# Kernel tuning notes

Hardware: AMD Instinct MI355X
Metric: run time of the kernel (lower is better)

The kernel has to match this reference:

```python
import jax, jax.numpy as jnp
import numpy as np

MARGIN = 0.2
LAMBDA_LSE = 6.0
LAMBDA_SOFTMAX = 9.0
EPS = 1e-8


def setup_inputs() -> dict:
    key = jax.random.key(0)
    k1, k2, k3 = jax.random.split(key, 3)
    I, R, W, D = 128, 36, 24, 512
    images = jax.random.normal(k1, (I, R, D), dtype=jnp.float32)
    captions = jax.random.normal(k2, (I, W, D), dtype=jnp.float32)
    # ragged caption lengths in [4, 24]
    cap_lens = 4 + jax.random.randint(k3, (I,), 0, W - 3, dtype=jnp.int32)
    return {"images": images, "captions": captions, "cap_lens": cap_lens}


def _scan_t2i_loss(images, captions, cap_lens):
    # images: [I, R, D]; captions: [C, W, D]; cap_lens: [C]
    C, W, D = captions.shape
    wmask = jnp.arange(W)[None, :] < cap_lens[:, None]          # [C, W] valid-word mask

    # raw attention: bmm(context=images, query^T=caption) -> [C, I, R, W]
    attn = jnp.einsum('ird,cwd->cirw', images, captions)
    # clipped_l2norm: LeakyReLU(0.1) then l2-normalize over word axis;
    # zero padded words so norms match the per-caption sliced computation
    a = jnp.where(attn > 0, attn, 0.1 * attn) * wmask[:, None, None, :]
    a = a / (jnp.sqrt(jnp.sum(a * a, axis=3, keepdims=True)) + EPS)
    # softmax over regions (sourceL) with temperature lambda_softmax
    s = jax.nn.softmax(a * LAMBDA_SOFTMAX, axis=2)              # [C, I, R, W]
    # weighted context per word: [C, I, W, D]
    wei = jnp.einsum('cirw,ird->ciwd', s, images)

    cap = captions[:, None, :, :]                               # [C, 1, W, D]
    num = jnp.sum(cap * wei, axis=-1)                           # [C, I, W]
    den = jnp.clip(jnp.linalg.norm(cap, axis=-1) * jnp.linalg.norm(wei, axis=-1), EPS)
    cos = num / den                                             # [C, I, W]

    # LogSumExp aggregation over valid words
    neg = jnp.finfo(cos.dtype).min
    logits = jnp.where(wmask[:, None, :], cos * LAMBDA_LSE, neg)
    row_sim = jax.nn.logsumexp(logits, axis=-1) / LAMBDA_LSE    # [C, I]
    scores = row_sim.T                                          # [I, C] (image x caption)

    diag = jnp.diag(scores)[:, None]                            # [I, 1]
    cost_s = jnp.clip(MARGIN + scores - diag, 0.0)
    cost_im = jnp.clip(MARGIN + scores - diag.T, 0.0)
    eye = jnp.eye(scores.shape[0], dtype=bool)
    cost_s = jnp.where(eye, 0.0, cost_s)
    cost_im = jnp.where(eye, 0.0, cost_im)
    # max_violation=True: hardest negatives
    cost_s = jnp.max(cost_s, axis=1)
    cost_im = jnp.max(cost_im, axis=0)
    return jnp.sum(cost_s) + jnp.sum(cost_im)


def reference(images, captions, cap_lens):
    return _scan_t2i_loss(images, captions, cap_lens)
```

## Files before the change

### kernel.cpp

```cpp
#include <hip/hip_runtime.h>
#include <math.h>

#define I_N 128
#define C_N 128
#define R_N 36
#define W_N 24
#define D_N 512
#define M_N (I_N * R_N)
#define N_N (C_N * W_N)

typedef __attribute__((ext_vector_type(8))) short bf16x8;
typedef __attribute__((ext_vector_type(4))) float f32x4;
typedef __attribute__((ext_vector_type(8))) unsigned short u16x8;
typedef _Float16 f16x2 __attribute__((ext_vector_type(2)));
typedef __fp16 h16x2 __attribute__((ext_vector_type(2)));

__device__ inline float bf2f(unsigned short u) {
    return __uint_as_float(((unsigned int)u) << 16);
}
__device__ inline unsigned short f2bf(float f) {
    unsigned int u = __float_as_uint(f);
    u = (u + 0x7FFFu + ((u >> 16) & 1u)) >> 16;
    return (unsigned short)u;
}
__device__ inline void gload_lds16(const void* g, void* l) {
    __builtin_amdgcn_global_load_lds(
        (const __attribute__((address_space(1))) void*)g,
        (__attribute__((address_space(3))) void*)l, 16, 0, 0);
}

#if __has_builtin(__builtin_amdgcn_fdot2)
__device__ inline float fdot2f(f16x2 a, f16x2 b, float c) {
    return __builtin_amdgcn_fdot2(__builtin_bit_cast(h16x2, a),
                                  __builtin_bit_cast(h16x2, b), c, false);
}
#else
__device__ inline float fdot2f(f16x2 a, f16x2 b, float c) {
    return c + (float)a[0] * (float)b[0] + (float)a[1] * (float)b[1];
}
#endif

#if __has_builtin(__builtin_amdgcn_cvt_pkrtz)
__device__ inline f16x2 pkf16(float a, float b) {
    return __builtin_bit_cast(f16x2, __builtin_amdgcn_cvt_pkrtz(a, b));
}
#else
__device__ inline f16x2 pkf16(float a, float b) {
    f16x2 v; v[0] = (_Float16)a; v[1] = (_Float16)b; return v;
}
#endif

__global__ __launch_bounds__(256) void convert_kernel(const float* __restrict__ images,
                                                      const float* __restrict__ captions,
                                                      unsigned short* __restrict__ imgbf,
                                                      unsigned short* __restrict__ capbf,
                                                      float* __restrict__ capn) {
    const int bid = blockIdx.x;
    if (bid < 1152) {
        int idx = bid * 256 + threadIdx.x;
        float4 v0 = *(const float4*)(images + (size_t)idx * 8);
        float4 v1 = *(const float4*)(images + (size_t)idx * 8 + 4);
        u16x8 o;
        o[0] = f2bf(v0.x); o[1] = f2bf(v0.y); o[2] = f2bf(v0.z); o[3] = f2bf(v0.w);
        o[4] = f2bf(v1.x); o[5] = f2bf(v1.y); o[6] = f2bf(v1.z); o[7] = f2bf(v1.w);
        *(u16x8*)(imgbf + (size_t)idx * 8) = o;
    } else {
        const int crow = (bid - 1152) * 4 + (threadIdx.x >> 6);
        const int lane = threadIdx.x & 63;
        const float* p = captions + (size_t)crow * D_N + lane * 8;
        float4 v0 = *(const float4*)p;
        float4 v1 = *(const float4*)(p + 4);
        u16x8 o;
        o[0] = f2bf(v0.x); o[1] = f2bf(v0.y); o[2] = f2bf(v0.z); o[3] = f2bf(v0.w);
        o[4] = f2bf(v1.x); o[5] = f2bf(v1.y); o[6] = f2bf(v1.z); o[7] = f2bf(v1.w);
        *(u16x8*)(capbf + (size_t)crow * D_N + lane * 8) = o;
        float s = v0.x*v0.x + v0.y*v0.y + v0.z*v0.z + v0.w*v0.w
                + v1.x*v1.x + v1.y*v1.y + v1.z*v1.z + v1.w*v1.w;
        #pragma unroll
        for (int off = 32; off > 0; off >>= 1) s += __shfl_down(s, off);
        if (lane == 0) capn[crow] = sqrtf(s);
    }
}

__global__ __launch_bounds__(256) void gram_kernel(const float* __restrict__ images,
                                                   float* __restrict__ G) {
    __shared__ float tile[R_N][68];
    const int i = blockIdx.x;
    const float* img = images + (size_t)i * R_N * D_N;
    const int tid = threadIdx.x;
    const int t1 = (tid / 12) * 3;
    const int t2 = (tid % 12) * 3;
    const bool active = tid < 144;
    float acc[3][3] = {{0.f,0.f,0.f},{0.f,0.f,0.f},{0.f,0.f,0.f}};
    for (int k0 = 0; k0 < D_N; k0 += 64) {
        for (int idx = tid; idx < R_N * 16; idx += 256) {
            int r = idx / 16, k4 = idx % 16;
            float4 v = *(const float4*)(img + (size_t)r * D_N + k0 + k4 * 4);
            *(float4*)&tile[r][k4 * 4] = v;
        }
        __syncthreads();
        if (active) {
            #pragma unroll
            for (int k = 0; k < 64; k += 4) {
                float4 a0 = *(const float4*)&tile[t1 + 0][k];
                float4 a1 = *(const float4*)&tile[t1 + 1][k];
                float4 a2 = *(const float4*)&tile[t1 + 2][k];
                float4 b0 = *(const float4*)&tile[t2 + 0][k];
                float4 b1 = *(const float4*)&tile[t2 + 1][k];
                float4 b2 = *(const float4*)&tile[t2 + 2][k];
                acc[0][0] += a0.x*b0.x + a0.y*b0.y + a0.z*b0.z + a0.w*b0.w;
                acc[0][1] += a0.x*b1.x + a0.y*b1.y + a0.z*b1.z + a0.w*b1.w;
                acc[0][2] += a0.x*b2.x + a0.y*b2.y + a0.z*b2.z + a0.w*b2.w;
                acc[1][0] += a1.x*b0.x + a1.y*b0.y + a1.z*b0.z + a1.w*b0.w;
                acc[1][1] += a1.x*b1.x + a1.y*b1.y + a1.z*b1.z + a1.w*b1.w;
                acc[1][2] += a1.x*b2.x + a1.y*b2.y + a1.z*b2.z + a1.w*b2.w;
                acc[2][0] += a2.x*b0.x + a2.y*b0.y + a2.z*b0.z + a2.w*b0.w;
                acc[2][1] += a2.x*b1.x + a2.y*b1.y + a2.z*b1.z + a2.w*b1.w;
                acc[2][2] += a2.x*b2.x + a2.y*b2.y + a2.z*b2.z + a2.w*b2.w;
            }
        }
        __syncthreads();
    }
    if (active) {
        float* gp = G + (size_t)i * R_N * R_N;
        #pragma unroll
        for (int a = 0; a < 3; ++a)
            #pragma unroll
            for (int b = 0; b < 3; ++b)
                gp[(t1 + a) * R_N + (t2 + b)] = acc[a][b];
    }
}

#define BM 128
#define BN 128
#define BK 64
#define KT (D_N / BK)
#define GX (M_N / BM)
#define GY (N_N / BN)

__global__ __launch_bounds__(256) void attn_gemm_kernel(const unsigned short* __restrict__ A,
                                                        const unsigned short* __restrict__ B,
                                                        unsigned short* __restrict__ attn) {
    __shared__ unsigned short AsBuf[2][BM * BK];
    __shared__ unsigned short BsBuf[2][BN * BK];
    const int flat = blockIdx.y * GX + blockIdx.x;
    const int nf = (flat & 7) * (GX * GY / 8) + (flat >> 3);
    const int m0 = (nf % GX) * BM;
    const int n0 = (nf / GX) * BN;
    const int tid = threadIdx.x;
    const int lane = tid & 63;
    const int wid = tid >> 6;
    const int wr = wid >> 1, wc = wid & 1;
    const int fr = lane & 15;
    const int fk = lane >> 4;

    const int srow = tid >> 3;
    const int sslot = (tid & 7) ^ (srow & 7);
    const unsigned short* srcA = A + (size_t)(m0 + srow) * D_N + sslot * 8;
    const unsigned short* srcB = B + (size_t)(n0 + srow) * D_N + sslot * 8;
    const int ldst = tid * 16;

    f32x4 acc[4][4];
    #pragma unroll
    for (int m = 0; m < 4; ++m)
        #pragma unroll
        for (int n = 0; n < 4; ++n) acc[m][n] = (f32x4){0.f, 0.f, 0.f, 0.f};

    #define STAGE(t, buf)                                                          \
        {                                                                          \
            const unsigned short* _a = srcA + (t) * BK;                            \
            const unsigned short* _b = srcB + (t) * BK;                            \
            _Pragma("unroll")                                                      \
            for (int r = 0; r < 4; ++r) {                                          \
                gload_lds16(_a + (size_t)r * 32 * D_N, (char*)AsBuf[buf] + r * 4096 + ldst); \
                gload_lds16(_b + (size_t)r * 32 * D_N, (char*)BsBuf[buf] + r * 4096 + ldst); \
            }                                                                      \
        }

    STAGE(0, 0)
    STAGE(1, 1)
    asm volatile("s_waitcnt vmcnt(8)" ::: "memory");
    __builtin_amdgcn_sched_barrier(0);
    __builtin_amdgcn_s_barrier();
    __builtin_amdgcn_sched_barrier(0);

    #pragma unroll
    for (int t = 0; t < KT; ++t) {
        const int cur = t & 1;
        const unsigned short* As = AsBuf[cur];
        const unsigned short* Bs = BsBuf[cur];
        #pragma unroll
        for (int ks = 0; ks < 2; ++ks) {
            bf16x8 af[4], bfr[4];
            #pragma unroll
            for (int m = 0; m < 4; ++m) {
                int rl = wr * 64 + m * 16 + fr;
                int byt = rl * 128 + ((ks * 64 + fk * 16) ^ ((fr & 7) << 4));
                af[m] = *(const bf16x8*)((const char*)As + byt);
            }
            #pragma unroll
            for (int n = 0; n < 4; ++n) {
                int rl = wc * 64 + n * 16 + fr;
                int byt = rl * 128 + ((ks * 64 + fk * 16) ^ ((fr & 7) << 4));
                bfr[n] = *(const bf16x8*)((const char*)Bs + byt);
            }
            #pragma unroll
            for (int m = 0; m < 4; ++m)
                #pragma unroll
                for (int n = 0; n < 4; ++n)
                    acc[m][n] = __builtin_amdgcn_mfma_f32_16x16x32_bf16(af[m], bfr[n], acc[m][n], 0, 0, 0);
        }
        __builtin_amdgcn_sched_barrier(0);
        __builtin_amdgcn_s_barrier();
        __builtin_amdgcn_sched_barrier(0);
        if (t + 2 < KT) STAGE(t + 2, cur)
        if (t + 1 < KT) {
            if (t + 2 < KT) {
                asm volatile("s_waitcnt vmcnt(8)" ::: "memory");
            } else {
                asm volatile("s_waitcnt vmcnt(0)" ::: "memory");
            }
            __builtin_amdgcn_sched_barrier(0);
            __builtin_amdgcn_s_barrier();
            __builtin_amdgcn_sched_barrier(0);
        }
    }
    #undef STAGE

    #pragma unroll
    for (int m = 0; m < 4; ++m) {
        #pragma unroll
        for (int n = 0; n < 4; ++n) {
            #pragma unroll
            for (int j = 0; j < 4; ++j) {
                int row = m0 + wr * 64 + m * 16 + fk * 4 + j;
                int col = n0 + wc * 64 + n * 16 + fr;
                int i = row / R_N, r = row - i * R_N;
                int c = col / W_N, w = col - c * W_N;
                attn[(((size_t)i * C_N + c) * R_N + r) * W_N + w] = f2bf(acc[m][n][j]);
            }
        }
    }
}

#define CG 16
#define SCL9 12.98425537f

__global__ __launch_bounds__(192) void score_kernel(const unsigned short* __restrict__ attn,
                                                    const float* __restrict__ G,
                                                    const float* __restrict__ capn,
                                                    const int* __restrict__ cap_lens,
                                                    float* __restrict__ scores) {
    __shared__ unsigned short stage[CG * R_N * W_N];
    __shared__ unsigned int gsh2[R_N][20];
    __shared__ float scl_sh[CG * R_N];
    __shared__ float red[CG][W_N];
    __shared__ int len_sh[CG];
    const int i = blockIdx.x;
    const int c0 = blockIdx.y * CG;
    const int tid = threadIdx.x;

    if (tid < CG) len_sh[tid] = cap_lens[c0 + tid];
    const unsigned short* at = attn + ((size_t)i * C_N + c0) * R_N * W_N;
    for (int ch = tid; ch < CG * R_N * W_N / 8; ch += 192)
        *(u16x8*)&stage[ch * 8] = *(const u16x8*)(at + ch * 8);
    const float* gp = G + (size_t)i * R_N * R_N;
    for (int idx = tid; idx < R_N * 20; idx += 192) {
        int r = idx / 20, p = idx % 20;
        f16x2 v;
        if (p < 18) v = pkf16(gp[r * R_N + 2 * p], gp[r * R_N + 2 * p + 1]);
        else { v[0] = (_Float16)0.f; v[1] = (_Float16)0.f; }
        gsh2[r][p] = __builtin_bit_cast(unsigned int, v);
    }
    __syncthreads();

    for (int row = tid; row < CG * R_N; row += 192) {
        int cl = row / R_N;
        int len = len_sh[cl];
        const unsigned short* rp = &stage[row * W_N];
        u16x8 p0 = *(const u16x8*)&rp[0];
        u16x8 p1 = *(const u16x8*)&rp[8];
        u16x8 p2 = *(const u16x8*)&rp[16];
        float ss = 0.f;
        #pragma unroll
        for (int q = 0; q < 8; ++q) {
            float x0 = bf2f(p0[q]); x0 = x0 > 0.f ? x0 : 0.1f * x0; x0 = (q      < len) ? x0 : 0.f;
            float x1 = bf2f(p1[q]); x1 = x1 > 0.f ? x1 : 0.1f * x1; x1 = (q + 8  < len) ? x1 : 0.f;
            float x2 = bf2f(p2[q]); x2 = x2 > 0.f ? x2 : 0.1f * x2; x2 = (q + 16 < len) ? x2 : 0.f;
            ss += x0 * x0 + x1 * x1 + x2 * x2;
        }
        scl_sh[row] = SCL9 / (sqrtf(ss) + 1e-8f);
    }
    __syncthreads();

    {
        const int cl = tid / 12, w0 = (tid % 12) * 2;
        const int len = len_sh[cl];
        const bool va = w0 < len, vb = w0 + 1 < len;
        const unsigned short* sb = &stage[cl * R_N * W_N];
        const float* sclp = &scl_sh[cl * R_N];
        f16x2 epa[18], epb[18];
        float Z0 = 0.f, Z1 = 0.f, nu0 = 0.f, nu1 = 0.f;
        float ea_prev = 0.f, eb_prev = 0.f;
        #pragma unroll
        for (int r = 0; r < R_N; ++r) {
            unsigned int pr = *(const unsigned int*)&sb[r * W_N + w0];
            float ra = bf2f((unsigned short)(pr & 0xffffu));
            float rb = bf2f((unsigned short)(pr >> 16));
            float s = sclp[r];
            float xa = ra > 0.f ? ra : 0.1f * ra;
            float xb = rb > 0.f ? rb : 0.1f * rb;
            float la = va ? xa * s : 0.f;
            float lb = vb ? xb * s : 0.f;
            float ea = exp2f(la), eb = exp2f(lb);
            Z0 += ea; Z1 += eb;
            nu0 += ea * ra; nu1 += eb * rb;
            if (r & 1) {
                epa[r >> 1] = pkf16(ea_prev, ea);
                epb[r >> 1] = pkf16(eb_prev, eb);
            } else {
                ea_prev = ea; eb_prev = eb;
            }
        }
        float wna = 0.f, wnb = 0.f;
        #pragma unroll
        for (int r2 = 0; r2 < R_N; ++r2) {
            const uint4* g4 = (const uint4*)&gsh2[r2][0];
            uint4 q0 = g4[0], q1 = g4[1], q2 = g4[2], q3 = g4[3];
            uint2 q4 = *(const uint2*)&gsh2[r2][16];
            unsigned int gq[18] = {q0.x, q0.y, q0.z, q0.w,
                                   q1.x, q1.y, q1.z, q1.w,
                                   q2.x, q2.y, q2.z, q2.w,
                                   q3.x, q3.y, q3.z, q3.w,
                                   q4.x, q4.y};
            float t0a = 0.f, t0b = 0.f, t1a = 0.f, t1b = 0.f;
            #pragma unroll
            for (int p = 0; p < 18; ++p) {
                f16x2 g = __builtin_bit_cast(f16x2, gq[p]);
                if (p & 1) { t0b = fdot2f(g, epa[p], t0b); t1b = fdot2f(g, epb[p], t1b); }
                else       { t0a = fdot2f(g, epa[p], t0a); t1a = fdot2f(g, epb[p], t1a); }
            }
            float ta = t0a + t0b, tb = t1a + t1b;
            float e2a = (float)epa[r2 >> 1][r2 & 1];
            float e2b = (float)epb[r2 >> 1][r2 & 1];
            wna += ta * e2a;
            wnb += tb * e2b;
        }
        float iZ0 = 1.f / Z0, iZ1 = 1.f / Z1;
        float cna = capn[(c0 + cl) * W_N + w0];
        float cnb = capn[(c0 + cl) * W_N + w0 + 1];
        float dena = fmaxf(cna * sqrtf(fmaxf(wna, 0.f)) * iZ0, 1e-8f);
        float denb = fmaxf(cnb * sqrtf(fmaxf(wnb, 0.f)) * iZ1, 1e-8f);
        red[cl][w0]     = va ? (nu0 * iZ0) / dena * 6.0f : -3.4e38f;
        red[cl][w0 + 1] = vb ? (nu1 * iZ1) / denb * 6.0f : -3.4e38f;
    }
    __syncthreads();
    if (tid < CG) {
        float se = 0.f;
        #pragma unroll
        for (int w = 0; w < W_N; ++w) se += __expf(red[tid][w] - 6.0f);
        scores[(size_t)(c0 + tid) * I_N + i] = (__logf(se) + 6.0f) / 6.0f;
    }
}

__global__ __launch_bounds__(128) void final_kernel(const float* __restrict__ scores,
                                                    float* __restrict__ out) {
    __shared__ float diag[C_N];
    __shared__ float red[C_N];
    const int t = threadIdx.x;
    diag[t] = scores[t * C_N + t];
    __syncthreads();
    const float di = diag[t];
    float cs = 0.f, cim = 0.f;
    for (int k = 0; k < C_N; ++k) {
        if (k == t) continue;
        float vs = 0.2f + scores[k * C_N + t] - di;
        float vi = 0.2f + scores[t * C_N + k] - di;
        cs = fmaxf(cs, vs);
        cim = fmaxf(cim, vi);
    }
    red[t] = cs + cim;
    __syncthreads();
    #pragma unroll
    for (int off = 64; off > 0; off >>= 1) {
        if (t < off) red[t] += red[t + off];
        __syncthreads();
    }
    if (t == 0) out[0] = red[0];
}

extern "C" void kernel_launch(void* const* d_in, const int* in_sizes, int n_in,
                              void* d_out, int out_size, void* d_ws, size_t ws_size,
                              hipStream_t stream) {
    (void)in_sizes; (void)n_in; (void)out_size; (void)ws_size;
    const float* images = (const float*)d_in[0];
    const float* captions = (const float*)d_in[1];
    const int* cap_lens = (const int*)d_in[2];
    float* out = (float*)d_out;

    char* wsb = (char*)d_ws;
    size_t off = 0;
    auto alloc = [&](size_t bytes) -> char* {
        char* p = wsb + off;
        off += (bytes + 255) & ~(size_t)255;
        return p;
    };
    unsigned short* imgbf = (unsigned short*)alloc((size_t)M_N * D_N * 2);
    unsigned short* capbf = (unsigned short*)alloc((size_t)N_N * D_N * 2);
    float* Gw = (float*)alloc((size_t)I_N * R_N * R_N * 4);
    float* capn = (float*)alloc((size_t)C_N * W_N * 4);
    float* scores = (float*)alloc((size_t)C_N * I_N * 4);
    unsigned short* attn = (unsigned short*)alloc((size_t)I_N * C_N * R_N * W_N * 2);

    convert_kernel<<<1920, 256, 0, stream>>>(images, captions, imgbf, capbf, capn);
    gram_kernel<<<I_N, 256, 0, stream>>>(images, Gw);
    attn_gemm_kernel<<<dim3(GX, GY), 256, 0, stream>>>(imgbf, capbf, attn);
    score_kernel<<<dim3(I_N, C_N / CG), 192, 0, stream>>>(attn, Gw, capn, cap_lens, scores);
    final_kernel<<<1, 128, 0, stream>>>(scores, out);
}
```

Before: 129.6 us.

## Halve GEMM K-tile, raise occupancy, remap blocks, pre-pack Gram matrix as fp16

Halves the attention GEMM's K tile from 64 to 32, which halves LDS use, and adds a launch bound of 4 blocks per CU to raise occupancy. It also switches to a 1-D grid with an M-major block remap and a matching LDS swizzle. The Gram kernel now writes its result already packed as fp16 pairs, so the score kernel drops its shared-memory Gram staging and reads the packed rows straight from global memory. The trade-offs are more barriers per K step in the GEMM, possible register pressure from the occupancy bound, and uncached global reads in the score kernel's inner loop.

```diff
diff --git a/kernel.cpp b/kernel.cpp
--- a/kernel.cpp
+++ b/kernel.cpp
@@ -83,8 +83,9 @@
 }
 
 __global__ __launch_bounds__(256) void gram_kernel(const float* __restrict__ images,
-                                                   float* __restrict__ G) {
+                                                   unsigned int* __restrict__ G2) {
     __shared__ float tile[R_N][68];
+    __shared__ float gshf[R_N][R_N];
     const int i = blockIdx.x;
     const float* img = images + (size_t)i * R_N * D_N;
     const int tid = threadIdx.x;
@@ -122,31 +123,36 @@
         __syncthreads();
     }
     if (active) {
-        float* gp = G + (size_t)i * R_N * R_N;
         #pragma unroll
         for (int a = 0; a < 3; ++a)
             #pragma unroll
             for (int b = 0; b < 3; ++b)
-                gp[(t1 + a) * R_N + (t2 + b)] = acc[a][b];
+                gshf[t1 + a][t2 + b] = acc[a][b];
+    }
+    __syncthreads();
+    unsigned int* gp = G2 + (size_t)i * (R_N * 18);
+    for (int idx = tid; idx < R_N * 18; idx += 256) {
+        int r = idx / 18, p = idx % 18;
+        gp[idx] = __builtin_bit_cast(unsigned int, pkf16(gshf[r][2 * p], gshf[r][2 * p + 1]));
     }
 }
 
 #define BM 128
 #define BN 128
-#define BK 64
+#define BK 32
 #define KT (D_N / BK)
 #define GX (M_N / BM)
 #define GY (N_N / BN)
 
-__global__ __launch_bounds__(256) void attn_gemm_kernel(const unsigned short* __restrict__ A,
-                                                        const unsigned short* __restrict__ B,
-                                                        unsigned short* __restrict__ attn) {
+__global__ __launch_bounds__(256, 4) void attn_gemm_kernel(const unsigned short* __restrict__ A,
+                                                           const unsigned short* __restrict__ B,
+                                                           unsigned short* __restrict__ attn) {
     __shared__ unsigned short AsBuf[2][BM * BK];
     __shared__ unsigned short BsBuf[2][BN * BK];
-    const int flat = blockIdx.y * GX + blockIdx.x;
+    const int flat = blockIdx.x;
     const int nf = (flat & 7) * (GX * GY / 8) + (flat >> 3);
-    const int m0 = (nf % GX) * BM;
-    const int n0 = (nf / GX) * BN;
+    const int m0 = (nf / GY) * BM;
+    const int n0 = (nf % GY) * BN;
     const int tid = threadIdx.x;
     const int lane = tid & 63;
     const int wid = tid >> 6;
@@ -154,8 +160,8 @@
     const int fr = lane & 15;
     const int fk = lane >> 4;
 
-    const int srow = tid >> 3;
-    const int sslot = (tid & 7) ^ (srow & 7);
+    const int srow = tid >> 2;
+    const int sslot = (tid & 3) ^ (srow & 3);
     const unsigned short* srcA = A + (size_t)(m0 + srow) * D_N + sslot * 8;
     const unsigned short* srcB = B + (size_t)(n0 + srow) * D_N + sslot * 8;
     const int ldst = tid * 16;
@@ -166,20 +172,19 @@
         #pragma unroll
         for (int n = 0; n < 4; ++n) acc[m][n] = (f32x4){0.f, 0.f, 0.f, 0.f};
 
-    #define STAGE(t, buf)                                                          \
-        {                                                                          \
-            const unsigned short* _a = srcA + (t) * BK;                            \
-            const unsigned short* _b = srcB + (t) * BK;                            \
-            _Pragma("unroll")                                                      \
-            for (int r = 0; r < 4; ++r) {                                          \
-                gload_lds16(_a + (size_t)r * 32 * D_N, (char*)AsBuf[buf] + r * 4096 + ldst); \
-                gload_lds16(_b + (size_t)r * 32 * D_N, (char*)BsBuf[buf] + r * 4096 + ldst); \
-            }                                                                      \
+    #define STAGE(t, buf)                                                              \
+        {                                                                              \
+            const unsigned short* _a = srcA + (t) * BK;                                \
+            const unsigned short* _b = srcB + (t) * BK;                                \
+            gload_lds16(_a, (char*)AsBuf[buf] + ldst);                                 \
+            gload_lds16(_a + (size_t)64 * D_N, (char*)AsBuf[buf] + 4096 + ldst);       \
+            gload_lds16(_b, (char*)BsBuf[buf] + ldst);                                 \
+            gload_lds16(_b + (size_t)64 * D_N, (char*)BsBuf[buf] + 4096 + ldst);       \
         }
 
     STAGE(0, 0)
     STAGE(1, 1)
-    asm volatile("s_waitcnt vmcnt(8)" ::: "memory");
+    asm volatile("s_waitcnt vmcnt(4)" ::: "memory");
     __builtin_amdgcn_sched_barrier(0);
     __builtin_amdgcn_s_barrier();
     __builtin_amdgcn_sched_barrier(0);
@@ -189,34 +194,31 @@
         const int cur = t & 1;
         const unsigned short* As = AsBuf[cur];
         const unsigned short* Bs = BsBuf[cur];
-        #pragma unroll
-        for (int ks = 0; ks < 2; ++ks) {
-            bf16x8 af[4], bfr[4];
+        bf16x8 af[4], bfr[4];
+        #pragma unroll
+        for (int m = 0; m < 4; ++m) {
+            int rl = wr * 64 + m * 16 + fr;
+            int byt = rl * 64 + ((fk ^ (fr & 3)) << 4);
+            af[m] = *(const bf16x8*)((const char*)As + byt);
+        }
+        #pragma unroll
+        for (int n = 0; n < 4; ++n) {
+            int rl = wc * 64 + n * 16 + fr;
+            int byt = rl * 64 + ((fk ^ (fr & 3)) << 4);
+            bfr[n] = *(const bf16x8*)((const char*)Bs + byt);
+        }
+        #pragma unroll
+        for (int m = 0; m < 4; ++m)
             #pragma unroll
-            for (int m = 0; m < 4; ++m) {
-                int rl = wr * 64 + m * 16 + fr;
-                int byt = rl * 128 + ((ks * 64 + fk * 16) ^ ((fr & 7) << 4));
-                af[m] = *(const bf16x8*)((const char*)As + byt);
-            }
-            #pragma unroll
-            for (int n = 0; n < 4; ++n) {
-                int rl = wc * 64 + n * 16 + fr;
-                int byt = rl * 128 + ((ks * 64 + fk * 16) ^ ((fr & 7) << 4));
-                bfr[n] = *(const bf16x8*)((const char*)Bs + byt);
-            }
-            #pragma unroll
-            for (int m = 0; m < 4; ++m)
-                #pragma unroll
-                for (int n = 0; n < 4; ++n)
-                    acc[m][n] = __builtin_amdgcn_mfma_f32_16x16x32_bf16(af[m], bfr[n], acc[m][n], 0, 0, 0);
-        }
+            for (int n = 0; n < 4; ++n)
+                acc[m][n] = __builtin_amdgcn_mfma_f32_16x16x32_bf16(af[m], bfr[n], acc[m][n], 0, 0, 0);
         __builtin_amdgcn_sched_barrier(0);
         __builtin_amdgcn_s_barrier();
         __builtin_amdgcn_sched_barrier(0);
         if (t + 2 < KT) STAGE(t + 2, cur)
         if (t + 1 < KT) {
             if (t + 2 < KT) {
-                asm volatile("s_waitcnt vmcnt(8)" ::: "memory");
+                asm volatile("s_waitcnt vmcnt(4)" ::: "memory");
             } else {
                 asm volatile("s_waitcnt vmcnt(0)" ::: "memory");
             }
@@ -247,12 +249,11 @@
 #define SCL9 12.98425537f
 
 __global__ __launch_bounds__(192) void score_kernel(const unsigned short* __restrict__ attn,
-                                                    const float* __restrict__ G,
+                                                    const unsigned int* __restrict__ G2,
                                                     const float* __restrict__ capn,
                                                     const int* __restrict__ cap_lens,
                                                     float* __restrict__ scores) {
     __shared__ unsigned short stage[CG * R_N * W_N];
-    __shared__ unsigned int gsh2[R_N][20];
     __shared__ float scl_sh[CG * R_N];
     __shared__ float red[CG][W_N];
     __shared__ int len_sh[CG];
@@ -264,14 +265,6 @@
     const unsigned short* at = attn + ((size_t)i * C_N + c0) * R_N * W_N;
     for (int ch = tid; ch < CG * R_N * W_N / 8; ch += 192)
         *(u16x8*)&stage[ch * 8] = *(const u16x8*)(at + ch * 8);
-    const float* gp = G + (size_t)i * R_N * R_N;
-    for (int idx = tid; idx < R_N * 20; idx += 192) {
-        int r = idx / 20, p = idx % 20;
-        f16x2 v;
-        if (p < 18) v = pkf16(gp[r * R_N + 2 * p], gp[r * R_N + 2 * p + 1]);
-        else { v[0] = (_Float16)0.f; v[1] = (_Float16)0.f; }
-        gsh2[r][p] = __builtin_bit_cast(unsigned int, v);
-    }
     __syncthreads();
 
     for (int row = tid; row < CG * R_N; row += 192) {
@@ -299,6 +292,7 @@
         const bool va = w0 < len, vb = w0 + 1 < len;
         const unsigned short* sb = &stage[cl * R_N * W_N];
         const float* sclp = &scl_sh[cl * R_N];
+        const unsigned int* g2 = G2 + (size_t)i * (R_N * 18);
         f16x2 epa[18], epb[18];
         float Z0 = 0.f, Z1 = 0.f, nu0 = 0.f, nu1 = 0.f;
         float ea_prev = 0.f, eb_prev = 0.f;
@@ -325,18 +319,11 @@
         float wna = 0.f, wnb = 0.f;
         #pragma unroll
         for (int r2 = 0; r2 < R_N; ++r2) {
-            const uint4* g4 = (const uint4*)&gsh2[r2][0];
-            uint4 q0 = g4[0], q1 = g4[1], q2 = g4[2], q3 = g4[3];
-            uint2 q4 = *(const uint2*)&gsh2[r2][16];
-            unsigned int gq[18] = {q0.x, q0.y, q0.z, q0.w,
-                                   q1.x, q1.y, q1.z, q1.w,
-                                   q2.x, q2.y, q2.z, q2.w,
-                                   q3.x, q3.y, q3.z, q3.w,
-                                   q4.x, q4.y};
+            const unsigned int* grow = g2 + r2 * 18;
             float t0a = 0.f, t0b = 0.f, t1a = 0.f, t1b = 0.f;
             #pragma unroll
             for (int p = 0; p < 18; ++p) {
-                f16x2 g = __builtin_bit_cast(f16x2, gq[p]);
+                f16x2 g = __builtin_bit_cast(f16x2, grow[p]);
                 if (p & 1) { t0b = fdot2f(g, epa[p], t0b); t1b = fdot2f(g, epb[p], t1b); }
                 else       { t0a = fdot2f(g, epa[p], t0a); t1a = fdot2f(g, epb[p], t1a); }
             }
@@ -407,14 +394,14 @@
     };
     unsigned short* imgbf = (unsigned short*)alloc((size_t)M_N * D_N * 2);
     unsigned short* capbf = (unsigned short*)alloc((size_t)N_N * D_N * 2);
-    float* Gw = (float*)alloc((size_t)I_N * R_N * R_N * 4);
+    unsigned int* G2 = (unsigned int*)alloc((size_t)I_N * R_N * 18 * 4);
     float* capn = (float*)alloc((size_t)C_N * W_N * 4);
     float* scores = (float*)alloc((size_t)C_N * I_N * 4);
     unsigned short* attn = (unsigned short*)alloc((size_t)I_N * C_N * R_N * W_N * 2);
 
     convert_kernel<<<1920, 256, 0, stream>>>(images, captions, imgbf, capbf, capn);
-    gram_kernel<<<I_N, 256, 0, stream>>>(images, Gw);
-    attn_gemm_kernel<<<dim3(GX, GY), 256, 0, stream>>>(imgbf, capbf, attn);
-    score_kernel<<<dim3(I_N, C_N / CG), 192, 0, stream>>>(attn, Gw, capn, cap_lens, scores);
+    gram_kernel<<<I_N, 256, 0, stream>>>(images, G2);
+    attn_gemm_kernel<<<GX * GY, 256, 0, stream>>>(imgbf, capbf, attn);
+    score_kernel<<<dim3(I_N, C_N / CG), 192, 0, stream>>>(attn, G2, capn, cap_lens, scores);
     final_kernel<<<1, 128, 0, stream>>>(scores, out);
 }
```

Measured after the change: 146.5 us. 1.13x slower.
